# Kernel optimization log

Hardware: AMD Instinct MI355X
Metric: run time of the kernel (lower is better)

## Reference

```python
import jax, jax.numpy as jnp
import numpy as np

N_NODES = 10000
N_EDGES = 320000
D = 128
H = 4
C = 128
L = 2
NEG_SLOPE = 0.2
LN_EPS = 1e-5


def setup_inputs() -> dict:
    key = jax.random.key(0)
    ks = jax.random.split(key, 8)
    x = jax.random.normal(ks[0], (N_NODES, D), dtype=jnp.float32)
    edge_index = jax.random.randint(ks[1], (2, N_EDGES), 0, N_NODES, dtype=jnp.int64)
    # weights scaled ~Glorot to keep attention logits in a sane range
    Wl = jax.random.normal(ks[2], (L, D, H * C), dtype=jnp.float32) * 0.1
    Wr = jax.random.normal(ks[3], (L, D, H * C), dtype=jnp.float32) * 0.1
    att = jax.random.normal(ks[4], (L, H, C), dtype=jnp.float32) * 0.1
    return {
        "x": x,
        "edge_index": edge_index,
        "Wl": Wl,
        "bl": jnp.zeros((L, H * C), jnp.float32),
        "Wr": Wr,
        "br": jnp.zeros((L, H * C), jnp.float32),
        "att": att,
        "bias": jnp.zeros((L, D), jnp.float32),
        "ln_g": jnp.ones((L, D), jnp.float32),
        "ln_b": jnp.zeros((L, D), jnp.float32),
    }


def _gatv2_layer(x, src, dst, Wl, bl, Wr, br, att, b):
    """GATv2Conv (concat=False -> head mean), messages src->dst, softmax over dst."""
    n = x.shape[0]
    xl = (x @ Wl + bl).reshape(n, H, C)  # source transform
    xr = (x @ Wr + br).reshape(n, H, C)  # target transform
    s = jax.nn.leaky_relu(xl[src] + xr[dst], NEG_SLOPE)  # [E, H, C]
    e = jnp.einsum("ehc,hc->eh", s, att)  # attention logits [E, H]
    m = jax.ops.segment_max(e, dst, num_segments=n)  # stable softmax per dst segment
    ex = jnp.exp(e - m[dst])
    denom = jax.ops.segment_sum(ex, dst, num_segments=n)
    alpha = ex / denom[dst]  # [E, H]
    out = jax.ops.segment_sum(alpha[:, :, None] * xl[src], dst, num_segments=n)  # [N, H, C]
    return out.mean(axis=1) + b  # concat=False -> mean over heads, then bias


def _layer_norm(h, g, b):
    mu = h.mean(-1, keepdims=True)
    var = ((h - mu) ** 2).mean(-1, keepdims=True)
    return (h - mu) * jax.lax.rsqrt(var + LN_EPS) * g + b


def reference(x, edge_index, Wl, bl, Wr, br, att, bias, ln_g, ln_b):
    n = x.shape[0]
    loop = jnp.arange(n, dtype=edge_index.dtype)
    src = jnp.concatenate([edge_index[0], loop])  # add self-loops (PyG default)
    dst = jnp.concatenate([edge_index[1], loop])
    for i in range(L):
        h = _gatv2_layer(x, src, dst, Wl[i], bl[i], Wr[i], br[i], att[i], bias[i])
        x = h + x  # residual
        x = jax.nn.relu(_layer_norm(x, ln_g[i], ln_b[i]))
    return x
```

## Files before the change

kernel.cpp:

```cpp
#include <hip/hip_runtime.h>
#include <math.h>

#define N_NODES 10000
#define N_EDGES 320000
#define E_TOT   (N_EDGES + N_NODES)
#define NEG 0.2f

typedef short bf16x8 __attribute__((ext_vector_type(8)));
typedef float f32x4 __attribute__((ext_vector_type(4)));
typedef float f32x2 __attribute__((ext_vector_type(2)));

static __device__ __forceinline__ float4 ld4g(const float* p) { return *(const float4*)p; }

static __device__ __forceinline__ unsigned short f2b(float f) {
    unsigned u;
    __builtin_memcpy(&u, &f, 4);
    unsigned r = (u + 0x7fffu + ((u >> 16) & 1u)) >> 16;
    return (unsigned short)r;
}
static __device__ __forceinline__ float b2f(unsigned short u) {
    unsigned x = ((unsigned)u) << 16;
    float f;
    __builtin_memcpy(&f, &x, 4);
    return f;
}
static __device__ __forceinline__ f32x2 unpk(unsigned d) {
    f32x2 r;
    r.x = __uint_as_float(d << 16);
    r.y = __uint_as_float(d & 0xffff0000u);
    return r;
}

template <int CTRL>
static __device__ __forceinline__ float dpp_add_step(float x) {
    int y = __builtin_amdgcn_update_dpp(0, __float_as_int(x), CTRL, 0xf, 0xf, true);
    return x + __int_as_float(y);
}
static __device__ __forceinline__ float row_sum16(float x) {
    x = dpp_add_step<0x121>(x);
    x = dpp_add_step<0x122>(x);
    x = dpp_add_step<0x124>(x);
    x = dpp_add_step<0x128>(x);
    return x;
}

__global__ void detect_dtype_kernel(const int* __restrict__ ei, int* __restrict__ flag) {
    __shared__ int any;
    if (threadIdx.x == 0) any = 0;
    __syncthreads();
    int v = ei[2 * threadIdx.x + 1];
    if (v != 0) atomicOr(&any, 1);
    __syncthreads();
    if (threadIdx.x == 0) *flag = (any == 0) ? 1 : 0;
}

static __device__ __forceinline__ int load_edge(const int* ei, int is64, int idx) {
    if (is64) { const long long* e64 = (const long long*)ei; return (int)e64[idx]; }
    return ei[idx];
}

__global__ void count_deg_kernel(const int* __restrict__ ei, const int* __restrict__ flag,
                                 int* __restrict__ deg) {
    int i = blockIdx.x * blockDim.x + threadIdx.x;
    if (i >= E_TOT) return;
    int is64 = *flag;
    int dst = (i < N_EDGES) ? load_edge(ei, is64, N_EDGES + i) : (i - N_EDGES);
    atomicAdd(&deg[dst], 1);
}

__global__ __launch_bounds__(256) void scan_kernel(const int* __restrict__ deg,
                                                   int* __restrict__ row_ptr,
                                                   int* __restrict__ cursor) {
    __shared__ int sums[256];
    int tid = threadIdx.x;
    int base = tid * 40;
    int d40[40];
    int s = 0;
    if (base < N_NODES) {
#pragma unroll
        for (int q = 0; q < 10; ++q) {
            int4 v = *(const int4*)(deg + base + q * 4);
            d40[q * 4 + 0] = v.x; d40[q * 4 + 1] = v.y;
            d40[q * 4 + 2] = v.z; d40[q * 4 + 3] = v.w;
            s += v.x + v.y + v.z + v.w;
        }
    }
    sums[tid] = s;
    __syncthreads();
    int run = s;
    for (int off = 1; off < 256; off <<= 1) {
        int t = (tid >= off) ? sums[tid - off] : 0;
        __syncthreads();
        run += t;
        sums[tid] = run;
        __syncthreads();
    }
    int excl = run - s;
    if (base < N_NODES) {
        int acc = excl;
#pragma unroll
        for (int i = 0; i < 40; ++i) {
            row_ptr[base + i] = acc;
            cursor[base + i] = acc;
            acc += d40[i];
        }
    }
    if (tid == 255) row_ptr[N_NODES] = run;
}

__global__ void fill_csr_kernel(const int* __restrict__ ei, const int* __restrict__ flag,
                                int* __restrict__ cursor, int* __restrict__ csr_src) {
    int i = blockIdx.x * blockDim.x + threadIdx.x;
    if (i >= E_TOT) return;
    int is64 = *flag;
    int src, dst;
    if (i < N_EDGES) { src = load_edge(ei, is64, i); dst = load_edge(ei, is64, N_EDGES + i); }
    else { src = i - N_EDGES; dst = src; }
    int pos = atomicAdd(&cursor[dst], 1);
    csr_src[pos] = src;
}

__global__ void convert_x_kernel(const float* __restrict__ x, unsigned short* __restrict__ xb) {
    int i = (blockIdx.x * blockDim.x + threadIdx.x) * 4;
    if (i >= N_NODES * 128) return;
    float4 v = ld4g(x + i);
    ushort4 o = make_ushort4(f2b(v.x), f2b(v.y), f2b(v.z), f2b(v.w));
    *(ushort4*)(xb + i) = o;
}

__global__ void convert_wt_kernel(const float* __restrict__ Wl, const float* __restrict__ Wr,
                                  unsigned short* __restrict__ WT) {
    __shared__ float t[32][33];
    int l = blockIdx.z;
    unsigned short* dst = WT + (size_t)l * 1024 * 128;
    int tx = threadIdx.x, ty = threadIdx.y;
    int n0 = blockIdx.x * 32, k0 = blockIdx.y * 32;
    const float* S = ((n0 < 512) ? Wl : Wr) + (size_t)l * 65536;
    int nn0 = n0 & 511;
#pragma unroll
    for (int it = 0; it < 4; ++it) {
        int k = k0 + ty + it * 8;
        t[ty + it * 8][tx] = S[(size_t)k * 512 + nn0 + tx];
    }
    __syncthreads();
#pragma unroll
    for (int it = 0; it < 4; ++it) {
        int n = n0 + ty + it * 8;
        int k = k0 + tx;
        dst[(size_t)n * 128 + k] = f2b(t[tx][ty + it * 8]);
    }
}

__global__ __launch_bounds__(256) void gemm_mfma_kernel(const unsigned short* __restrict__ A,
                                                        const unsigned short* __restrict__ Bt,
                                                        const float* __restrict__ bl,
                                                        const float* __restrict__ br,
                                                        unsigned short* __restrict__ Y) {
    __shared__ unsigned short As[128][72];
    __shared__ unsigned short Bs[128][72];
    int tid = threadIdx.x;
    int wave = tid >> 6, lane = tid & 63;
    int wm = wave >> 1, wn = wave & 1;
    int l15 = lane & 15, quad = lane >> 4;
    int row0 = blockIdx.y * 128, col0 = blockIdx.x * 128;
    const float* bias = (col0 < 512) ? (bl + col0) : (br + col0 - 512);

    f32x4 acc[4][4];
#pragma unroll
    for (int mi = 0; mi < 4; ++mi)
#pragma unroll
        for (int ni = 0; ni < 4; ++ni)
#pragma unroll
            for (int r = 0; r < 4; ++r) acc[mi][ni][r] = 0.f;

#pragma unroll
    for (int kc = 0; kc < 2; ++kc) {
#pragma unroll
        for (int it = 0; it < 4; ++it) {
            int e = tid + it * 256;
            int r = e >> 3, s = e & 7;
            int gr = row0 + r;
            bf16x8 v = (bf16x8)(short)0;
            if (gr < N_NODES) v = *(const bf16x8*)(A + (size_t)gr * 128 + kc * 64 + s * 8);
            *(bf16x8*)&As[r][s * 8] = v;
            bf16x8 w = *(const bf16x8*)(Bt + (size_t)(col0 + r) * 128 + kc * 64 + s * 8);
            *(bf16x8*)&Bs[r][s * 8] = w;
        }
        __syncthreads();
#pragma unroll
        for (int kq = 0; kq < 2; ++kq) {
            bf16x8 af[4], bfr[4];
#pragma unroll
            for (int mi = 0; mi < 4; ++mi)
                af[mi] = *(const bf16x8*)&As[wm * 64 + mi * 16 + l15][kq * 32 + quad * 8];
#pragma unroll
            for (int ni = 0; ni < 4; ++ni)
                bfr[ni] = *(const bf16x8*)&Bs[wn * 64 + ni * 16 + l15][kq * 32 + quad * 8];
#pragma unroll
            for (int mi = 0; mi < 4; ++mi)
#pragma unroll
                for (int ni = 0; ni < 4; ++ni)
                    acc[mi][ni] = __builtin_amdgcn_mfma_f32_16x16x32_bf16(af[mi], bfr[ni], acc[mi][ni], 0, 0, 0);
        }
        __syncthreads();
    }

    float bv[4];
#pragma unroll
    for (int ni = 0; ni < 4; ++ni) bv[ni] = bias[wn * 64 + ni * 16 + l15];

#pragma unroll
    for (int mi = 0; mi < 4; ++mi) {
#pragma unroll
        for (int r = 0; r < 4; ++r) {
            int grow = row0 + wm * 64 + mi * 16 + quad * 4 + r;
            if (grow >= N_NODES) continue;
#pragma unroll
            for (int ni = 0; ni < 4; ++ni) {
                int gcol = col0 + wn * 64 + ni * 16 + l15;
                Y[(size_t)grow * 1024 + gcol] = f2b(acc[mi][ni][r] + bv[ni]);
            }
        }
    }
}

__global__ __launch_bounds__(256) void attn_kernel(
    const unsigned short* __restrict__ xlr,
    const float* __restrict__ x_in, const int* __restrict__ row_ptr,
    const int* __restrict__ csr_src, const float* __restrict__ att,
    const float* __restrict__ bias, const float* __restrict__ ln_g,
    const float* __restrict__ ln_b, float* __restrict__ x_out,
    unsigned short* __restrict__ xb_out) {
    int wave = (blockIdx.x * blockDim.x + threadIdx.x) >> 6;
    int lane = threadIdx.x & 63;
    if (wave >= N_NODES) return;
    int dst = wave;
    int g = lane & 15;
    int off = 8 * lane;

    f32x2 xr2[4], at2[4];
    {
        uint4 u = *(const uint4*)(xlr + (size_t)dst * 1024 + 512 + off);
        xr2[0] = unpk(u.x); xr2[1] = unpk(u.y); xr2[2] = unpk(u.z); xr2[3] = unpk(u.w);
        float4 a = ld4g(att + off);
        float4 b = ld4g(att + off + 4);
        at2[0].x = a.x; at2[0].y = a.y; at2[1].x = a.z; at2[1].y = a.w;
        at2[2].x = b.x; at2[2].y = b.y; at2[3].x = b.z; at2[3].y = b.w;
    }
    const f32x2 neg2 = {NEG, NEG};

    float d = 0.f;
    f32x2 acc2[4] = {{0.f, 0.f}, {0.f, 0.f}, {0.f, 0.f}, {0.f, 0.f}};

    int beg = row_ptr[dst], end = row_ptr[dst + 1];
    int nfull = (end - beg) & ~3;
    int pend = beg + nfull;
    int p = beg;

    if (nfull) {
        int s0 = csr_src[p], s1 = csr_src[p + 1], s2 = csr_src[p + 2], s3 = csr_src[p + 3];
        uint4 u0 = *(const uint4*)(xlr + (size_t)s0 * 1024 + off);
        uint4 u1 = *(const uint4*)(xlr + (size_t)s1 * 1024 + off);
        uint4 u2 = *(const uint4*)(xlr + (size_t)s2 * 1024 + off);
        uint4 u3 = *(const uint4*)(xlr + (size_t)s3 * 1024 + off);
        while (true) {
            p += 4;
            bool more = p < pend;
            uint4 n0, n1, n2, n3;
            if (more) {
                int t0 = csr_src[p], t1 = csr_src[p + 1], t2 = csr_src[p + 2], t3 = csr_src[p + 3];
                n0 = *(const uint4*)(xlr + (size_t)t0 * 1024 + off);
                n1 = *(const uint4*)(xlr + (size_t)t1 * 1024 + off);
                n2 = *(const uint4*)(xlr + (size_t)t2 * 1024 + off);
                n3 = *(const uint4*)(xlr + (size_t)t3 * 1024 + off);
            }
            const unsigned* w0 = (const unsigned*)&u0;
            const unsigned* w1 = (const unsigned*)&u1;
            const unsigned* w2 = (const unsigned*)&u2;
            const unsigned* w3 = (const unsigned*)&u3;
            f32x2 q0 = {0.f, 0.f}, q1 = {0.f, 0.f}, q2 = {0.f, 0.f}, q3 = {0.f, 0.f};
#pragma unroll
            for (int q = 0; q < 4; ++q) {
                f32x2 s;
                s = unpk(w0[q]) + xr2[q]; s = __builtin_elementwise_max(s, s * neg2);
                q0 = __builtin_elementwise_fma(s, at2[q], q0);
                s = unpk(w1[q]) + xr2[q]; s = __builtin_elementwise_max(s, s * neg2);
                q1 = __builtin_elementwise_fma(s, at2[q], q1);
                s = unpk(w2[q]) + xr2[q]; s = __builtin_elementwise_max(s, s * neg2);
                q2 = __builtin_elementwise_fma(s, at2[q], q2);
                s = unpk(w3[q]) + xr2[q]; s = __builtin_elementwise_max(s, s * neg2);
                q3 = __builtin_elementwise_fma(s, at2[q], q3);
            }
            float p0 = row_sum16(q0.x + q0.y);
            float p1 = row_sum16(q1.x + q1.y);
            float p2 = row_sum16(q2.x + q2.y);
            float p3 = row_sum16(q3.x + q3.y);
            float e0 = __expf(p0), e1 = __expf(p1), e2 = __expf(p2), e3 = __expf(p3);
            d += (e0 + e1) + (e2 + e3);
            f32x2 W0 = {e0, e0}, W1 = {e1, e1}, W2 = {e2, e2}, W3 = {e3, e3};
#pragma unroll
            for (int q = 0; q < 4; ++q) {
                f32x2 t = __builtin_elementwise_fma(unpk(w0[q]), W0, acc2[q]);
                t = __builtin_elementwise_fma(unpk(w1[q]), W1, t);
                t = __builtin_elementwise_fma(unpk(w2[q]), W2, t);
                acc2[q] = __builtin_elementwise_fma(unpk(w3[q]), W3, t);
            }
            if (!more) break;
            u0 = n0; u1 = n1; u2 = n2; u3 = n3;
        }
    }
    for (; p < end; ++p) {
        int s0 = csr_src[p];
        uint4 u0 = *(const uint4*)(xlr + (size_t)s0 * 1024 + off);
        const unsigned* w0 = (const unsigned*)&u0;
        f32x2 q0 = {0.f, 0.f};
#pragma unroll
        for (int q = 0; q < 4; ++q) {
            f32x2 s = unpk(w0[q]) + xr2[q];
            s = __builtin_elementwise_max(s, s * neg2);
            q0 = __builtin_elementwise_fma(s, at2[q], q0);
        }
        float p0 = row_sum16(q0.x + q0.y);
        float e0 = __expf(p0);
        d += e0;
        f32x2 W0 = {e0, e0};
#pragma unroll
        for (int q = 0; q < 4; ++q)
            acc2[q] = __builtin_elementwise_fma(unpk(w0[q]), W0, acc2[q]);
    }

    float inv = 1.f / d;
    float t[8];
#pragma unroll
    for (int q = 0; q < 4; ++q) {
        t[2 * q] = acc2[q].x * inv;
        t[2 * q + 1] = acc2[q].y * inv;
    }
#pragma unroll
    for (int j = 0; j < 8; ++j) {
        t[j] += __shfl_xor(t[j], 16, 64);
        t[j] += __shfl_xor(t[j], 32, 64);
    }
    float4 bi0 = ld4g(bias + 8 * g), bi1 = ld4g(bias + 8 * g + 4);
    float4 xi0 = ld4g(x_in + (size_t)dst * 128 + 8 * g);
    float4 xi1 = ld4g(x_in + (size_t)dst * 128 + 8 * g + 4);
    float hc[8];
    hc[0] = t[0] * 0.25f + bi0.x + xi0.x;
    hc[1] = t[1] * 0.25f + bi0.y + xi0.y;
    hc[2] = t[2] * 0.25f + bi0.z + xi0.z;
    hc[3] = t[3] * 0.25f + bi0.w + xi0.w;
    hc[4] = t[4] * 0.25f + bi1.x + xi1.x;
    hc[5] = t[5] * 0.25f + bi1.y + xi1.y;
    hc[6] = t[6] * 0.25f + bi1.z + xi1.z;
    hc[7] = t[7] * 0.25f + bi1.w + xi1.w;

    float sm = 0.f, sq = 0.f;
#pragma unroll
    for (int j = 0; j < 8; ++j) { sm += hc[j]; sq = fmaf(hc[j], hc[j], sq); }
    sm = row_sum16(sm);
    sq = row_sum16(sq);
    float mu = sm * (1.f / 128.f);
    float var = sq * (1.f / 128.f) - mu * mu;
    float rs = rsqrtf(var + 1e-5f);
    float4 g0 = ld4g(ln_g + 8 * g), g1 = ld4g(ln_g + 8 * g + 4);
    float4 b0 = ld4g(ln_b + 8 * g), b1 = ld4g(ln_b + 8 * g + 4);
    float y[8];
    y[0] = fmaxf((hc[0] - mu) * rs * g0.x + b0.x, 0.f);
    y[1] = fmaxf((hc[1] - mu) * rs * g0.y + b0.y, 0.f);
    y[2] = fmaxf((hc[2] - mu) * rs * g0.z + b0.z, 0.f);
    y[3] = fmaxf((hc[3] - mu) * rs * g0.w + b0.w, 0.f);
    y[4] = fmaxf((hc[4] - mu) * rs * g1.x + b1.x, 0.f);
    y[5] = fmaxf((hc[5] - mu) * rs * g1.y + b1.y, 0.f);
    y[6] = fmaxf((hc[6] - mu) * rs * g1.z + b1.z, 0.f);
    y[7] = fmaxf((hc[7] - mu) * rs * g1.w + b1.w, 0.f);

    if (lane < 16) {
        float4 o0 = make_float4(y[0], y[1], y[2], y[3]);
        float4 o1 = make_float4(y[4], y[5], y[6], y[7]);
        *(float4*)(x_out + (size_t)dst * 128 + 8 * g) = o0;
        *(float4*)(x_out + (size_t)dst * 128 + 8 * g + 4) = o1;
        if (xb_out) {
            ushort4 c0 = make_ushort4(f2b(y[0]), f2b(y[1]), f2b(y[2]), f2b(y[3]));
            ushort4 c1 = make_ushort4(f2b(y[4]), f2b(y[5]), f2b(y[6]), f2b(y[7]));
            *(ushort4*)(xb_out + (size_t)dst * 128 + 8 * g) = c0;
            *(ushort4*)(xb_out + (size_t)dst * 128 + 8 * g + 4) = c1;
        }
    }
}

extern "C" void kernel_launch(void* const* d_in, const int* in_sizes, int n_in,
                              void* d_out, int out_size, void* d_ws, size_t ws_size,
                              hipStream_t stream) {
    const float* x    = (const float*)d_in[0];
    const int*   ei   = (const int*)d_in[1];
    const float* Wl   = (const float*)d_in[2];
    const float* bl   = (const float*)d_in[3];
    const float* Wr   = (const float*)d_in[4];
    const float* br   = (const float*)d_in[5];
    const float* att  = (const float*)d_in[6];
    const float* bias = (const float*)d_in[7];
    const float* lng  = (const float*)d_in[8];
    const float* lnb  = (const float*)d_in[9];
    float* out = (float*)d_out;

    char* ws = (char*)d_ws;
    unsigned short* xlr = (unsigned short*)ws; ws += (size_t)N_NODES * 1024 * 2;
    float* xbuf  = (float*)ws;          ws += (size_t)N_NODES * 128 * 4;
    unsigned short* xb = (unsigned short*)ws; ws += (size_t)N_NODES * 128 * 2;
    unsigned short* WT = (unsigned short*)ws; ws += (size_t)2 * 1024 * 128 * 2;
    int* deg     = (int*)ws;            ws += (size_t)N_NODES * 4;
    int* row_ptr = (int*)ws;            ws += (size_t)(N_NODES + 4) * 4;
    int* cursor  = (int*)ws;            ws += (size_t)N_NODES * 4;
    int* csr_src = (int*)ws;            ws += (size_t)E_TOT * 4;
    int* flag    = (int*)ws;            ws += 256;

    hipMemsetAsync(deg, 0, N_NODES * sizeof(int), stream);
    detect_dtype_kernel<<<1, 256, 0, stream>>>(ei, flag);
    count_deg_kernel<<<(E_TOT + 255) / 256, 256, 0, stream>>>(ei, flag, deg);
    scan_kernel<<<1, 256, 0, stream>>>(deg, row_ptr, cursor);
    fill_csr_kernel<<<(E_TOT + 255) / 256, 256, 0, stream>>>(ei, flag, cursor, csr_src);

    convert_wt_kernel<<<dim3(32, 4, 2), dim3(32, 8), 0, stream>>>(Wl, Wr, WT);
    convert_x_kernel<<<(N_NODES * 128 / 4 + 255) / 256, 256, 0, stream>>>(x, xb);

    for (int l = 0; l < 2; ++l) {
        const float* xin = (l == 0) ? x : xbuf;
        float* xout = (l == 0) ? xbuf : out;
        unsigned short* xbo = (l == 0) ? xb : (unsigned short*)nullptr;
        gemm_mfma_kernel<<<dim3(8, 79), 256, 0, stream>>>(xb, WT + (size_t)l * 1024 * 128, bl + (size_t)l * 512,
                                                          br + (size_t)l * 512, xlr);
        attn_kernel<<<(N_NODES * 64 + 255) / 256, 256, 0, stream>>>(
            xlr, xin, row_ptr, csr_src,
            att + (size_t)l * 512, bias + (size_t)l * 128,
            lng + (size_t)l * 128, lnb + (size_t)l * 128, xout, xbo);
    }
}
```

Before: 247.3 us.

## Split each destination's edge list across two waves and combine partials in LDS

Each destination node's incoming edges are split in half between two waves of the block, and the second wave's partial accumulators and softmax denominator are merged into the first through shared memory before the epilogue. This doubles the number of waves issuing gather loads per node, giving more memory-level parallelism for the latency-bound neighbour gathers. The bf16 unpack is also hoisted so each loaded value is converted once and reused for both the logit and the accumulation. Costs are a block-wide barrier, LDS traffic, and half the waves sitting idle through the epilogue. Without a running max, splitting the sum stays exact.

```diff
diff --git a/kernel.cpp b/kernel.cpp
--- a/kernel.cpp
+++ b/kernel.cpp
@@ -231,10 +231,11 @@
     const float* __restrict__ bias, const float* __restrict__ ln_g,
     const float* __restrict__ ln_b, float* __restrict__ x_out,
     unsigned short* __restrict__ xb_out) {
-    int wave = (blockIdx.x * blockDim.x + threadIdx.x) >> 6;
+    int wid = threadIdx.x >> 6;
     int lane = threadIdx.x & 63;
-    if (wave >= N_NODES) return;
-    int dst = wave;
+    int pair = wid >> 1;
+    int half = wid & 1;
+    int dst = blockIdx.x * 2 + pair;
     int g = lane & 15;
     int off = 8 * lane;
 
@@ -253,9 +254,14 @@
     f32x2 acc2[4] = {{0.f, 0.f}, {0.f, 0.f}, {0.f, 0.f}, {0.f, 0.f}};
 
     int beg = row_ptr[dst], end = row_ptr[dst + 1];
-    int nfull = (end - beg) & ~3;
-    int pend = beg + nfull;
-    int p = beg;
+    int len = end - beg;
+    int h0 = (len + 1) >> 1;
+    int b = half ? (beg + h0) : beg;
+    int e = half ? end : (beg + h0);
+
+    int nfull = (e - b) & ~3;
+    int pend = b + nfull;
+    int p = b;
 
     if (nfull) {
         int s0 = csr_src[p], s1 = csr_src[p + 1], s2 = csr_src[p + 2], s3 = csr_src[p + 3];
@@ -274,21 +280,29 @@
                 n2 = *(const uint4*)(xlr + (size_t)t2 * 1024 + off);
                 n3 = *(const uint4*)(xlr + (size_t)t3 * 1024 + off);
             }
-            const unsigned* w0 = (const unsigned*)&u0;
-            const unsigned* w1 = (const unsigned*)&u1;
-            const unsigned* w2 = (const unsigned*)&u2;
-            const unsigned* w3 = (const unsigned*)&u3;
+            f32x2 F0[4], F1[4], F2[4], F3[4];
+            {
+                const unsigned* w0 = (const unsigned*)&u0;
+                const unsigned* w1 = (const unsigned*)&u1;
+                const unsigned* w2 = (const unsigned*)&u2;
+                const unsigned* w3 = (const unsigned*)&u3;
+#pragma unroll
+                for (int q = 0; q < 4; ++q) {
+                    F0[q] = unpk(w0[q]); F1[q] = unpk(w1[q]);
+                    F2[q] = unpk(w2[q]); F3[q] = unpk(w3[q]);
+                }
+            }
             f32x2 q0 = {0.f, 0.f}, q1 = {0.f, 0.f}, q2 = {0.f, 0.f}, q3 = {0.f, 0.f};
 #pragma unroll
             for (int q = 0; q < 4; ++q) {
                 f32x2 s;
-                s = unpk(w0[q]) + xr2[q]; s = __builtin_elementwise_max(s, s * neg2);
+                s = F0[q] + xr2[q]; s = __builtin_elementwise_max(s, s * neg2);
                 q0 = __builtin_elementwise_fma(s, at2[q], q0);
-                s = unpk(w1[q]) + xr2[q]; s = __builtin_elementwise_max(s, s * neg2);
+                s = F1[q] + xr2[q]; s = __builtin_elementwise_max(s, s * neg2);
                 q1 = __builtin_elementwise_fma(s, at2[q], q1);
-                s = unpk(w2[q]) + xr2[q]; s = __builtin_elementwise_max(s, s * neg2);
+                s = F2[q] + xr2[q]; s = __builtin_elementwise_max(s, s * neg2);
                 q2 = __builtin_elementwise_fma(s, at2[q], q2);
-                s = unpk(w3[q]) + xr2[q]; s = __builtin_elementwise_max(s, s * neg2);
+                s = F3[q] + xr2[q]; s = __builtin_elementwise_max(s, s * neg2);
                 q3 = __builtin_elementwise_fma(s, at2[q], q3);
             }
             float p0 = row_sum16(q0.x + q0.y);
@@ -300,23 +314,26 @@
             f32x2 W0 = {e0, e0}, W1 = {e1, e1}, W2 = {e2, e2}, W3 = {e3, e3};
 #pragma unroll
             for (int q = 0; q < 4; ++q) {
-                f32x2 t = __builtin_elementwise_fma(unpk(w0[q]), W0, acc2[q]);
-                t = __builtin_elementwise_fma(unpk(w1[q]), W1, t);
-                t = __builtin_elementwise_fma(unpk(w2[q]), W2, t);
-                acc2[q] = __builtin_elementwise_fma(unpk(w3[q]), W3, t);
+                f32x2 t = __builtin_elementwise_fma(F0[q], W0, acc2[q]);
+                t = __builtin_elementwise_fma(F1[q], W1, t);
+                t = __builtin_elementwise_fma(F2[q], W2, t);
+                acc2[q] = __builtin_elementwise_fma(F3[q], W3, t);
             }
             if (!more) break;
             u0 = n0; u1 = n1; u2 = n2; u3 = n3;
         }
     }
-    for (; p < end; ++p) {
+    for (; p < e; ++p) {
         int s0 = csr_src[p];
         uint4 u0 = *(const uint4*)(xlr + (size_t)s0 * 1024 + off);
         const unsigned* w0 = (const unsigned*)&u0;
+        f32x2 F0[4];
+#pragma unroll
+        for (int q = 0; q < 4; ++q) F0[q] = unpk(w0[q]);
         f32x2 q0 = {0.f, 0.f};
 #pragma unroll
         for (int q = 0; q < 4; ++q) {
-            f32x2 s = unpk(w0[q]) + xr2[q];
+            f32x2 s = F0[q] + xr2[q];
             s = __builtin_elementwise_max(s, s * neg2);
             q0 = __builtin_elementwise_fma(s, at2[q], q0);
         }
@@ -326,8 +343,24 @@
         f32x2 W0 = {e0, e0};
 #pragma unroll
         for (int q = 0; q < 4; ++q)
-            acc2[q] = __builtin_elementwise_fma(unpk(w0[q]), W0, acc2[q]);
-    }
+            acc2[q] = __builtin_elementwise_fma(F0[q], W0, acc2[q]);
+    }
+
+    __shared__ float pa[2][64][9];
+    if (half) {
+        pa[pair][lane][0] = acc2[0].x; pa[pair][lane][1] = acc2[0].y;
+        pa[pair][lane][2] = acc2[1].x; pa[pair][lane][3] = acc2[1].y;
+        pa[pair][lane][4] = acc2[2].x; pa[pair][lane][5] = acc2[2].y;
+        pa[pair][lane][6] = acc2[3].x; pa[pair][lane][7] = acc2[3].y;
+        pa[pair][lane][8] = d;
+    }
+    __syncthreads();
+    if (half) return;
+    acc2[0].x += pa[pair][lane][0]; acc2[0].y += pa[pair][lane][1];
+    acc2[1].x += pa[pair][lane][2]; acc2[1].y += pa[pair][lane][3];
+    acc2[2].x += pa[pair][lane][4]; acc2[2].y += pa[pair][lane][5];
+    acc2[3].x += pa[pair][lane][6]; acc2[3].y += pa[pair][lane][7];
+    d += pa[pair][lane][8];
 
     float inv = 1.f / d;
     float t[8];
@@ -429,7 +462,7 @@
         unsigned short* xbo = (l == 0) ? xb : (unsigned short*)nullptr;
         gemm_mfma_kernel<<<dim3(8, 79), 256, 0, stream>>>(xb, WT + (size_t)l * 1024 * 128, bl + (size_t)l * 512,
                                                           br + (size_t)l * 512, xlr);
-        attn_kernel<<<(N_NODES * 64 + 255) / 256, 256, 0, stream>>>(
+        attn_kernel<<<N_NODES / 2, 256, 0, stream>>>(
             xlr, xin, row_ptr, csr_src,
             att + (size_t)l * 512, bias + (size_t)l * 128,
             lng + (size_t)l * 128, lnb + (size_t)l * 128, xout, xbo);
```

Result: no change. 248.9 us (+0.7%).

## Fuse CSR build and conversions into one cooperative kernel; prefetch indices

Applied to the files above, without the earlier changes.

The memset plus six separate prep kernels (dtype detection, degree count, scan, CSR fill, x and weight conversion) are replaced by a single cooperative kernel with grid-wide syncs, cutting launch overhead and inter-kernel gaps. Separately, the attention loop now prefetches the next group's CSR indices one iteration ahead and unpacks bf16 values once into registers for reuse. The cooperative launch needs all 512 blocks to be co-resident, and grid.sync adds its own barrier cost. The extra unpacked registers may raise register pressure in the attention kernel.

```diff
diff --git a/kernel.cpp b/kernel.cpp
--- a/kernel.cpp
+++ b/kernel.cpp
@@ -1,10 +1,14 @@
 #include <hip/hip_runtime.h>
+#include <hip/hip_cooperative_groups.h>
 #include <math.h>
+
+namespace cg = cooperative_groups;
 
 #define N_NODES 10000
 #define N_EDGES 320000
 #define E_TOT   (N_EDGES + N_NODES)
 #define NEG 0.2f
+#define PREP_BLOCKS 512
 
 typedef short bf16x8 __attribute__((ext_vector_type(8)));
 typedef float f32x4 __attribute__((ext_vector_type(4)));
@@ -17,12 +21,6 @@
     __builtin_memcpy(&u, &f, 4);
     unsigned r = (u + 0x7fffu + ((u >> 16) & 1u)) >> 16;
     return (unsigned short)r;
-}
-static __device__ __forceinline__ float b2f(unsigned short u) {
-    unsigned x = ((unsigned)u) << 16;
-    float f;
-    __builtin_memcpy(&f, &x, 4);
-    return f;
 }
 static __device__ __forceinline__ f32x2 unpk(unsigned d) {
     f32x2 r;
@@ -44,110 +42,109 @@
     return x;
 }
 
-__global__ void detect_dtype_kernel(const int* __restrict__ ei, int* __restrict__ flag) {
-    __shared__ int any;
-    if (threadIdx.x == 0) any = 0;
-    __syncthreads();
-    int v = ei[2 * threadIdx.x + 1];
-    if (v != 0) atomicOr(&any, 1);
-    __syncthreads();
-    if (threadIdx.x == 0) *flag = (any == 0) ? 1 : 0;
-}
-
 static __device__ __forceinline__ int load_edge(const int* ei, int is64, int idx) {
     if (is64) { const long long* e64 = (const long long*)ei; return (int)e64[idx]; }
     return ei[idx];
 }
 
-__global__ void count_deg_kernel(const int* __restrict__ ei, const int* __restrict__ flag,
-                                 int* __restrict__ deg) {
-    int i = blockIdx.x * blockDim.x + threadIdx.x;
-    if (i >= E_TOT) return;
+__global__ __launch_bounds__(256) void prep_kernel(
+    const float* __restrict__ x, const int* __restrict__ ei,
+    const float* __restrict__ Wl, const float* __restrict__ Wr,
+    unsigned short* __restrict__ xb, unsigned short* __restrict__ WT,
+    int* __restrict__ deg, int* __restrict__ row_ptr, int* __restrict__ cursor,
+    int* __restrict__ csr_src, int* __restrict__ flag) {
+    cg::grid_group grid = cg::this_grid();
+    int tid = threadIdx.x, bid = blockIdx.x;
+    int gtid = bid * 256 + tid;
+    int gstride = PREP_BLOCKS * 256;
+
+    __shared__ float tbuf[32][33];
+    __shared__ int sums[256];
+    __shared__ int any;
+
+    for (int i = gtid; i < N_NODES; i += gstride) deg[i] = 0;
+    if (bid == PREP_BLOCKS - 1) {
+        if (tid == 0) any = 0;
+        __syncthreads();
+        if (ei[2 * tid + 1] != 0) atomicOr(&any, 1);
+        __syncthreads();
+        if (tid == 0) *flag = (any == 0) ? 1 : 0;
+    }
+    for (int i = gtid; i < N_NODES * 32; i += gstride) {
+        float4 v = ld4g(x + 4 * i);
+        ushort4 o = make_ushort4(f2b(v.x), f2b(v.y), f2b(v.z), f2b(v.w));
+        *(ushort4*)(xb + 4 * i) = o;
+    }
+    if (bid < 256) {
+        int l = bid >> 7;
+        int rest = bid & 127;
+        int ky = rest >> 5, nx = rest & 31;
+        int n0 = nx * 32, k0 = ky * 32;
+        const float* S = ((n0 < 512) ? Wl : Wr) + (size_t)l * 65536;
+        int nn0 = n0 & 511;
+        int tx = tid & 31, ty = tid >> 5;
+#pragma unroll
+        for (int it = 0; it < 4; ++it) {
+            int k = k0 + ty + it * 8;
+            tbuf[ty + it * 8][tx] = S[(size_t)k * 512 + nn0 + tx];
+        }
+        __syncthreads();
+        unsigned short* dstp = WT + (size_t)l * 1024 * 128;
+#pragma unroll
+        for (int it = 0; it < 4; ++it) {
+            int n = n0 + ty + it * 8;
+            int k = k0 + tx;
+            dstp[(size_t)n * 128 + k] = f2b(tbuf[tx][ty + it * 8]);
+        }
+    }
+    grid.sync();
+
     int is64 = *flag;
-    int dst = (i < N_EDGES) ? load_edge(ei, is64, N_EDGES + i) : (i - N_EDGES);
-    atomicAdd(&deg[dst], 1);
-}
-
-__global__ __launch_bounds__(256) void scan_kernel(const int* __restrict__ deg,
-                                                   int* __restrict__ row_ptr,
-                                                   int* __restrict__ cursor) {
-    __shared__ int sums[256];
-    int tid = threadIdx.x;
-    int base = tid * 40;
-    int d40[40];
-    int s = 0;
-    if (base < N_NODES) {
-#pragma unroll
-        for (int q = 0; q < 10; ++q) {
-            int4 v = *(const int4*)(deg + base + q * 4);
-            d40[q * 4 + 0] = v.x; d40[q * 4 + 1] = v.y;
-            d40[q * 4 + 2] = v.z; d40[q * 4 + 3] = v.w;
-            s += v.x + v.y + v.z + v.w;
-        }
-    }
-    sums[tid] = s;
-    __syncthreads();
-    int run = s;
-    for (int off = 1; off < 256; off <<= 1) {
-        int t = (tid >= off) ? sums[tid - off] : 0;
-        __syncthreads();
-        run += t;
-        sums[tid] = run;
-        __syncthreads();
-    }
-    int excl = run - s;
-    if (base < N_NODES) {
-        int acc = excl;
-#pragma unroll
-        for (int i = 0; i < 40; ++i) {
-            row_ptr[base + i] = acc;
-            cursor[base + i] = acc;
-            acc += d40[i];
-        }
-    }
-    if (tid == 255) row_ptr[N_NODES] = run;
-}
-
-__global__ void fill_csr_kernel(const int* __restrict__ ei, const int* __restrict__ flag,
-                                int* __restrict__ cursor, int* __restrict__ csr_src) {
-    int i = blockIdx.x * blockDim.x + threadIdx.x;
-    if (i >= E_TOT) return;
-    int is64 = *flag;
-    int src, dst;
-    if (i < N_EDGES) { src = load_edge(ei, is64, i); dst = load_edge(ei, is64, N_EDGES + i); }
-    else { src = i - N_EDGES; dst = src; }
-    int pos = atomicAdd(&cursor[dst], 1);
-    csr_src[pos] = src;
-}
-
-__global__ void convert_x_kernel(const float* __restrict__ x, unsigned short* __restrict__ xb) {
-    int i = (blockIdx.x * blockDim.x + threadIdx.x) * 4;
-    if (i >= N_NODES * 128) return;
-    float4 v = ld4g(x + i);
-    ushort4 o = make_ushort4(f2b(v.x), f2b(v.y), f2b(v.z), f2b(v.w));
-    *(ushort4*)(xb + i) = o;
-}
-
-__global__ void convert_wt_kernel(const float* __restrict__ Wl, const float* __restrict__ Wr,
-                                  unsigned short* __restrict__ WT) {
-    __shared__ float t[32][33];
-    int l = blockIdx.z;
-    unsigned short* dst = WT + (size_t)l * 1024 * 128;
-    int tx = threadIdx.x, ty = threadIdx.y;
-    int n0 = blockIdx.x * 32, k0 = blockIdx.y * 32;
-    const float* S = ((n0 < 512) ? Wl : Wr) + (size_t)l * 65536;
-    int nn0 = n0 & 511;
-#pragma unroll
-    for (int it = 0; it < 4; ++it) {
-        int k = k0 + ty + it * 8;
-        t[ty + it * 8][tx] = S[(size_t)k * 512 + nn0 + tx];
-    }
-    __syncthreads();
-#pragma unroll
-    for (int it = 0; it < 4; ++it) {
-        int n = n0 + ty + it * 8;
-        int k = k0 + tx;
-        dst[(size_t)n * 128 + k] = f2b(t[tx][ty + it * 8]);
+    for (int i = gtid; i < E_TOT; i += gstride) {
+        int dst = (i < N_EDGES) ? load_edge(ei, is64, N_EDGES + i) : (i - N_EDGES);
+        atomicAdd(&deg[dst], 1);
+    }
+    grid.sync();
+
+    if (bid == 0) {
+        int base = tid * 40;
+        int s = 0;
+        if (base < N_NODES) {
+#pragma unroll
+            for (int i = 0; i < 40; i += 4) {
+                int4 v = *(const int4*)(deg + base + i);
+                s += v.x + v.y + v.z + v.w;
+            }
+        }
+        sums[tid] = s;
+        __syncthreads();
+        int run = s;
+        for (int off = 1; off < 256; off <<= 1) {
+            int t = (tid >= off) ? sums[tid - off] : 0;
+            __syncthreads();
+            run += t;
+            sums[tid] = run;
+            __syncthreads();
+        }
+        if (base < N_NODES) {
+            int acc = run - s;
+            for (int i = 0; i < 40; ++i) {
+                int dv = deg[base + i];
+                row_ptr[base + i] = acc;
+                cursor[base + i] = acc;
+                acc += dv;
+            }
+        }
+        if (tid == 255) row_ptr[N_NODES] = run;
+    }
+    grid.sync();
+
+    for (int i = gtid; i < E_TOT; i += gstride) {
+        int src, dst;
+        if (i < N_EDGES) { src = load_edge(ei, is64, i); dst = load_edge(ei, is64, N_EDGES + i); }
+        else { src = i - N_EDGES; dst = src; }
+        int pos = atomicAdd(&cursor[dst], 1);
+        csr_src[pos] = src;
     }
 }
 
@@ -258,37 +255,51 @@
     int p = beg;
 
     if (nfull) {
-        int s0 = csr_src[p], s1 = csr_src[p + 1], s2 = csr_src[p + 2], s3 = csr_src[p + 3];
-        uint4 u0 = *(const uint4*)(xlr + (size_t)s0 * 1024 + off);
-        uint4 u1 = *(const uint4*)(xlr + (size_t)s1 * 1024 + off);
-        uint4 u2 = *(const uint4*)(xlr + (size_t)s2 * 1024 + off);
-        uint4 u3 = *(const uint4*)(xlr + (size_t)s3 * 1024 + off);
+        int i0 = csr_src[p], i1 = csr_src[p + 1], i2 = csr_src[p + 2], i3 = csr_src[p + 3];
+        uint4 u0 = *(const uint4*)(xlr + (size_t)i0 * 1024 + off);
+        uint4 u1 = *(const uint4*)(xlr + (size_t)i1 * 1024 + off);
+        uint4 u2 = *(const uint4*)(xlr + (size_t)i2 * 1024 + off);
+        uint4 u3 = *(const uint4*)(xlr + (size_t)i3 * 1024 + off);
+        if (p + 4 < pend) {
+            i0 = csr_src[p + 4]; i1 = csr_src[p + 5]; i2 = csr_src[p + 6]; i3 = csr_src[p + 7];
+        }
         while (true) {
             p += 4;
             bool more = p < pend;
             uint4 n0, n1, n2, n3;
             if (more) {
-                int t0 = csr_src[p], t1 = csr_src[p + 1], t2 = csr_src[p + 2], t3 = csr_src[p + 3];
-                n0 = *(const uint4*)(xlr + (size_t)t0 * 1024 + off);
-                n1 = *(const uint4*)(xlr + (size_t)t1 * 1024 + off);
-                n2 = *(const uint4*)(xlr + (size_t)t2 * 1024 + off);
-                n3 = *(const uint4*)(xlr + (size_t)t3 * 1024 + off);
-            }
-            const unsigned* w0 = (const unsigned*)&u0;
-            const unsigned* w1 = (const unsigned*)&u1;
-            const unsigned* w2 = (const unsigned*)&u2;
-            const unsigned* w3 = (const unsigned*)&u3;
+                n0 = *(const uint4*)(xlr + (size_t)i0 * 1024 + off);
+                n1 = *(const uint4*)(xlr + (size_t)i1 * 1024 + off);
+                n2 = *(const uint4*)(xlr + (size_t)i2 * 1024 + off);
+                n3 = *(const uint4*)(xlr + (size_t)i3 * 1024 + off);
+                if (p + 4 < pend) {
+                    i0 = csr_src[p + 4]; i1 = csr_src[p + 5];
+                    i2 = csr_src[p + 6]; i3 = csr_src[p + 7];
+                }
+            }
+            f32x2 F0[4], F1[4], F2[4], F3[4];
+            {
+                const unsigned* w0 = (const unsigned*)&u0;
+                const unsigned* w1 = (const unsigned*)&u1;
+                const unsigned* w2 = (const unsigned*)&u2;
+                const unsigned* w3 = (const unsigned*)&u3;
+#pragma unroll
+                for (int q = 0; q < 4; ++q) {
+                    F0[q] = unpk(w0[q]); F1[q] = unpk(w1[q]);
+                    F2[q] = unpk(w2[q]); F3[q] = unpk(w3[q]);
+                }
+            }
             f32x2 q0 = {0.f, 0.f}, q1 = {0.f, 0.f}, q2 = {0.f, 0.f}, q3 = {0.f, 0.f};
 #pragma unroll
             for (int q = 0; q < 4; ++q) {
                 f32x2 s;
-                s = unpk(w0[q]) + xr2[q]; s = __builtin_elementwise_max(s, s * neg2);
+                s = F0[q] + xr2[q]; s = __builtin_elementwise_max(s, s * neg2);
                 q0 = __builtin_elementwise_fma(s, at2[q], q0);
-                s = unpk(w1[q]) + xr2[q]; s = __builtin_elementwise_max(s, s * neg2);
+                s = F1[q] + xr2[q]; s = __builtin_elementwise_max(s, s * neg2);
                 q1 = __builtin_elementwise_fma(s, at2[q], q1);
-                s = unpk(w2[q]) + xr2[q]; s = __builtin_elementwise_max(s, s * neg2);
+                s = F2[q] + xr2[q]; s = __builtin_elementwise_max(s, s * neg2);
                 q2 = __builtin_elementwise_fma(s, at2[q], q2);
-                s = unpk(w3[q]) + xr2[q]; s = __builtin_elementwise_max(s, s * neg2);
+                s = F3[q] + xr2[q]; s = __builtin_elementwise_max(s, s * neg2);
                 q3 = __builtin_elementwise_fma(s, at2[q], q3);
             }
             float p0 = row_sum16(q0.x + q0.y);
@@ -300,10 +311,10 @@
             f32x2 W0 = {e0, e0}, W1 = {e1, e1}, W2 = {e2, e2}, W3 = {e3, e3};
 #pragma unroll
             for (int q = 0; q < 4; ++q) {
-                f32x2 t = __builtin_elementwise_fma(unpk(w0[q]), W0, acc2[q]);
-                t = __builtin_elementwise_fma(unpk(w1[q]), W1, t);
-                t = __builtin_elementwise_fma(unpk(w2[q]), W2, t);
-                acc2[q] = __builtin_elementwise_fma(unpk(w3[q]), W3, t);
+                f32x2 t = __builtin_elementwise_fma(F0[q], W0, acc2[q]);
+                t = __builtin_elementwise_fma(F1[q], W1, t);
+                t = __builtin_elementwise_fma(F2[q], W2, t);
+                acc2[q] = __builtin_elementwise_fma(F3[q], W3, t);
             }
             if (!more) break;
             u0 = n0; u1 = n1; u2 = n2; u3 = n3;
@@ -313,10 +324,13 @@
         int s0 = csr_src[p];
         uint4 u0 = *(const uint4*)(xlr + (size_t)s0 * 1024 + off);
         const unsigned* w0 = (const unsigned*)&u0;
+        f32x2 F0[4];
+#pragma unroll
+        for (int q = 0; q < 4; ++q) F0[q] = unpk(w0[q]);
         f32x2 q0 = {0.f, 0.f};
 #pragma unroll
         for (int q = 0; q < 4; ++q) {
-            f32x2 s = unpk(w0[q]) + xr2[q];
+            f32x2 s = F0[q] + xr2[q];
             s = __builtin_elementwise_max(s, s * neg2);
             q0 = __builtin_elementwise_fma(s, at2[q], q0);
         }
@@ -326,7 +340,7 @@
         f32x2 W0 = {e0, e0};
 #pragma unroll
         for (int q = 0; q < 4; ++q)
-            acc2[q] = __builtin_elementwise_fma(unpk(w0[q]), W0, acc2[q]);
+            acc2[q] = __builtin_elementwise_fma(F0[q], W0, acc2[q]);
     }
 
     float inv = 1.f / d;
@@ -414,20 +428,20 @@
     int* csr_src = (int*)ws;            ws += (size_t)E_TOT * 4;
     int* flag    = (int*)ws;            ws += 256;
 
-    hipMemsetAsync(deg, 0, N_NODES * sizeof(int), stream);
-    detect_dtype_kernel<<<1, 256, 0, stream>>>(ei, flag);
-    count_deg_kernel<<<(E_TOT + 255) / 256, 256, 0, stream>>>(ei, flag, deg);
-    scan_kernel<<<1, 256, 0, stream>>>(deg, row_ptr, cursor);
-    fill_csr_kernel<<<(E_TOT + 255) / 256, 256, 0, stream>>>(ei, flag, cursor, csr_src);
-
-    convert_wt_kernel<<<dim3(32, 4, 2), dim3(32, 8), 0, stream>>>(Wl, Wr, WT);
-    convert_x_kernel<<<(N_NODES * 128 / 4 + 255) / 256, 256, 0, stream>>>(x, xb);
+    {
+        void* args[] = {(void*)&x, (void*)&ei, (void*)&Wl, (void*)&Wr,
+                        (void*)&xb, (void*)&WT, (void*)&deg, (void*)&row_ptr,
+                        (void*)&cursor, (void*)&csr_src, (void*)&flag};
+        hipLaunchCooperativeKernel((void*)prep_kernel, dim3(PREP_BLOCKS), dim3(256),
+                                   args, 0, stream);
+    }
 
     for (int l = 0; l < 2; ++l) {
         const float* xin = (l == 0) ? x : xbuf;
         float* xout = (l == 0) ? xbuf : out;
         unsigned short* xbo = (l == 0) ? xb : (unsigned short*)nullptr;
-        gemm_mfma_kernel<<<dim3(8, 79), 256, 0, stream>>>(xb, WT + (size_t)l * 1024 * 128, bl + (size_t)l * 512,
+        gemm_mfma_kernel<<<dim3(8, 79), 256, 0, stream>>>(xb, WT + (size_t)l * 1024 * 128,
+                                                          bl + (size_t)l * 512,
                                                           br + (size_t)l * 512, xlr);
         attn_kernel<<<(N_NODES * 64 + 255) / 256, 256, 0, stream>>>(
             xlr, xin, row_ptr, csr_src,
```

Measured after the change: 425.4 us. 72.0% more time.
